# Optimization experiments

Hardware: AMD Instinct MI355X
Metric: run time of the kernel (lower is better)

Reference implementation:

```python
import jax, jax.numpy as jnp
import numpy as np

N, E, D, H, C = 50000, 1600000, 128, 2, 32

def setup_inputs() -> dict:
    key = jax.random.key(0)
    ks = jax.random.split(key, 8)
    x = jax.random.normal(ks[0], (N, D), jnp.float32)
    edge_index = jax.random.randint(ks[1], (2, E), 0, N)
    intra_enrichment_weights = jax.random.uniform(ks[2], (E,), jnp.float32)
    W = jax.random.normal(ks[3], (D, H * C), jnp.float32) * (1.0 / np.sqrt(D))
    att_src = jax.random.normal(ks[4], (H, C), jnp.float32) * 0.1
    att_dst = jax.random.normal(ks[5], (H, C), jnp.float32) * 0.1
    bias = jnp.zeros((H * C,), jnp.float32)
    enrichment_scale = jnp.asarray(0.01, jnp.float32)
    return dict(x=x, edge_index=edge_index,
                intra_enrichment_weights=intra_enrichment_weights,
                W=W, att_src=att_src, att_dst=att_dst, bias=bias,
                enrichment_scale=enrichment_scale)

def reference(x, edge_index, intra_enrichment_weights, W, att_src, att_dst, bias, enrichment_scale):
    n = x.shape[0]
    xf = jax.nn.elu(x)                       # F.elu on input features
    h = (xf @ W).reshape(n, H, C)            # [N, heads, out]
    # GATConv default add_self_loops=True
    loop = jnp.arange(n, dtype=edge_index.dtype)
    src = jnp.concatenate([edge_index[0], loop])
    dst = jnp.concatenate([edge_index[1], loop])
    a_src = jnp.einsum('nhc,hc->nh', h, att_src)   # [N, H]
    a_dst = jnp.einsum('nhc,hc->nh', h, att_dst)
    alpha = jax.nn.leaky_relu(a_src[src] + a_dst[dst], 0.2)  # [E+N, H]
    # softmax over incoming edges per destination node
    m = jax.ops.segment_max(alpha, dst, num_segments=n)
    e = jnp.exp(alpha - m[dst])
    denom = jax.ops.segment_sum(e, dst, num_segments=n)
    p = e / denom[dst]                       # every node has a self-loop -> denom > 0
    out = jax.ops.segment_sum(h[src] * p[:, :, None], dst, num_segments=n)  # [N, H, C]
    out = out.reshape(n, H * C) + bias
    # enrichment bias (scatter-mean of per-edge weights over source nodes)
    s0 = edge_index[0]
    nw = jax.ops.segment_sum(intra_enrichment_weights, s0, num_segments=n)
    cnt = jax.ops.segment_sum(jnp.ones_like(intra_enrichment_weights), s0, num_segments=n)
    nw = nw / jnp.maximum(cnt, 1.0)
    nw = jnp.clip(nw, 0.2, 5.0)
    scale_factor = 0.1 * jax.nn.sigmoid(enrichment_scale)
    return out + scale_factor * (nw[:, None] - 1.0)
```

## Files before the change

kernel.cpp:

```cpp
#include <hip/hip_runtime.h>


typedef unsigned int u32;
typedef unsigned short u16;

#define SLOTS 4864
#define NB_MAX 400
#define EPB 4096

#define XS 136
#define CS 68

typedef __attribute__((ext_vector_type(8))) short short8;
typedef __attribute__((ext_vector_type(4))) float float4v;

__device__ __forceinline__ u16 f2bf(float f) {
    union { float f; u32 u; } v; v.f = f;
    u32 r = v.u + 0x7fffu + ((v.u >> 16) & 1u);
    return (u16)(r >> 16);
}
__device__ __forceinline__ float bf2f(u16 u) {
    union { u32 i; float f; } v; v.i = ((u32)u) << 16; return v.f;
}
__device__ __forceinline__ float bf_lo(u32 u) {
    union { u32 i; float f; } v; v.i = u << 16; return v.f;
}
__device__ __forceinline__ float bf_hi(u32 u) {
    union { u32 i; float f; } v; v.i = u & 0xFFFF0000u; return v.f;
}
__device__ __forceinline__ void bf_split(float v, short& hi, short& lo) {
    u16 h = f2bf(v);
    float hf = bf2f(h);
    hi = (short)h;
    lo = (short)f2bf(v - hf);
}

__global__ void k_init(int* cursA, int* cursB, int nb) {
    int t = threadIdx.x;
    if (t < nb) { cursA[t] = 0; cursB[t] = 0; }
}

__global__ __launch_bounds__(256) void k_node(
    const float* __restrict__ x, const float* __restrict__ Wm,
    const float* __restrict__ att_s, const float* __restrict__ att_d,
    u32* __restrict__ hb32, float* __restrict__ a_src, float* __restrict__ a_dst,
    int nN)
{
    __shared__ __align__(16) short Ah[64 * XS];
    __shared__ __align__(16) short Al[64 * XS];
    __shared__ __align__(16) short Bh[64 * XS];
    __shared__ __align__(16) short Bl[64 * XS];
    float* Cl = (float*)Ah;

    int t = threadIdx.x;
    int n0 = blockIdx.x * 64;

    {
        int f = t & 63, kq = t >> 6;
        for (int kk = 0; kk < 32; ++kk) {
            int k = kq * 32 + kk;
            float wv = Wm[k * 64 + f];
            short hi, lo; bf_split(wv, hi, lo);
            Bh[f * XS + k] = hi; Bl[f * XS + k] = lo;
        }
    }
    for (int j = 0; j < 8; ++j) {
        int idx = t + 256 * j;
        int r = idx >> 5, c4 = idx & 31;
        int gn = n0 + r;
        float4 xv = make_float4(0.f, 0.f, 0.f, 0.f);
        if (gn < nN) xv = ((const float4*)x)[(size_t)gn * 32 + c4];
        float e[4];
        e[0] = xv.x > 0.f ? xv.x : expm1f(xv.x);
        e[1] = xv.y > 0.f ? xv.y : expm1f(xv.y);
        e[2] = xv.z > 0.f ? xv.z : expm1f(xv.z);
        e[3] = xv.w > 0.f ? xv.w : expm1f(xv.w);
        short h4[4], l4[4];
#pragma unroll
        for (int i = 0; i < 4; ++i) bf_split(e[i], h4[i], l4[i]);
        *(short4*)&Ah[r * XS + c4 * 4] = make_short4(h4[0], h4[1], h4[2], h4[3]);
        *(short4*)&Al[r * XS + c4 * 4] = make_short4(l4[0], l4[1], l4[2], l4[3]);
    }
    __syncthreads();

    {
        int w = t >> 6, l = t & 63;
        int q = l >> 4, m = l & 15;
        int arow = w * 16 + m;
        float4v acc[4] = {};
#pragma unroll
        for (int ks = 0; ks < 4; ++ks) {
            int k0 = ks * 32 + q * 8;
            short8 ah = *(const short8*)&Ah[arow * XS + k0];
            short8 al = *(const short8*)&Al[arow * XS + k0];
#pragma unroll
            for (int nt = 0; nt < 4; ++nt) {
                short8 bh = *(const short8*)&Bh[(nt * 16 + m) * XS + k0];
                short8 bl = *(const short8*)&Bl[(nt * 16 + m) * XS + k0];
                acc[nt] = __builtin_amdgcn_mfma_f32_16x16x32_bf16(ah, bh, acc[nt], 0, 0, 0);
                acc[nt] = __builtin_amdgcn_mfma_f32_16x16x32_bf16(ah, bl, acc[nt], 0, 0, 0);
                acc[nt] = __builtin_amdgcn_mfma_f32_16x16x32_bf16(al, bh, acc[nt], 0, 0, 0);
            }
        }
        __syncthreads();
#pragma unroll
        for (int nt = 0; nt < 4; ++nt)
#pragma unroll
            for (int r = 0; r < 4; ++r)
                Cl[(w * 16 + q * 4 + r) * CS + nt * 16 + m] = acc[nt][r];
    }
    __syncthreads();

    {
        int nl = t >> 2, fq = t & 3;
        int gn = n0 + nl;
        float ps = 0.f, pd = 0.f;
        if (gn < nN) {
            float hv[16];
#pragma unroll
            for (int i = 0; i < 16; ++i) {
                int f = fq * 16 + i;
                hv[i] = Cl[nl * CS + f];
                ps = fmaf(hv[i], att_s[f], ps);
                pd = fmaf(hv[i], att_d[f], pd);
            }
#pragma unroll
            for (int i = 0; i < 8; ++i) {
                u32 pk = ((u32)f2bf(hv[2 * i + 1]) << 16) | (u32)f2bf(hv[2 * i]);
                hb32[(size_t)gn * 32 + fq * 8 + i] = pk;
            }
        }
        float ps2 = ps + __shfl_xor(ps, 1, 64);
        float pd2 = pd + __shfl_xor(pd, 1, 64);
        if (gn < nN && (fq & 1) == 0) {
            a_src[2 * gn + (fq >> 1)] = ps2;
            a_dst[2 * gn + (fq >> 1)] = pd2;
        }
    }
}

__global__ __launch_bounds__(256) void k_partA(
    const int* __restrict__ ei, const float* __restrict__ wgt,
    int* cursA, int* cursB, u32* bufA, u32* bufB, int E, int nb)
{
    __shared__ u32 arrA[EPB], arrB[EPB];
    __shared__ u16 bkA[EPB], bkB[EPB];
    __shared__ int cntA[NB_MAX], cntB[NB_MAX];
    __shared__ int lofsA[NB_MAX], lofsB[NB_MAX];
    __shared__ int basA[NB_MAX], basB[NB_MAX];
    __shared__ int part[256];

    int t = threadIdx.x;
    for (int b = t; b < nb; b += 256) { cntA[b] = 0; cntB[b] = 0; }
    __syncthreads();

    int base = blockIdx.x * EPB;
    int nv = min(EPB, E - base);
    int sv[16], dv[16]; float wv[16];
#pragma unroll
    for (int k = 0; k < 16; ++k) {
        int e = base + k * 256 + t;
        if (e < E) { sv[k] = ei[e]; dv[k] = ei[E + e]; wv[k] = wgt[e]; }
        else       { sv[k] = -1;    dv[k] = -1;        wv[k] = 0.f; }
    }
#pragma unroll
    for (int k = 0; k < 16; ++k) {
        if (dv[k] >= 0) {
            atomicAdd(&cntA[dv[k] >> 7], 1);
            atomicAdd(&cntB[sv[k] >> 7], 1);
        }
    }
    __syncthreads();
    for (int b = t; b < nb; b += 256) {
        int ca = cntA[b], cb = cntB[b];
        if (ca > 0) basA[b] = atomicAdd(&cursA[b], ca);
        if (cb > 0) basB[b] = atomicAdd(&cursB[b], cb);
    }
    __syncthreads();
    {
        int b0 = 2 * t, b1 = 2 * t + 1;
        int c0 = (b0 < nb) ? cntA[b0] : 0;
        int c1 = (b1 < nb) ? cntA[b1] : 0;
        part[t] = c0 + c1;
        __syncthreads();
        for (int off = 1; off < 256; off <<= 1) {
            int v = (t >= off) ? part[t - off] : 0;
            __syncthreads();
            part[t] += v;
            __syncthreads();
        }
        int excl = part[t] - (c0 + c1);
        if (b0 < nb) lofsA[b0] = excl;
        if (b1 < nb) lofsA[b1] = excl + c0;
        __syncthreads();
        c0 = (b0 < nb) ? cntB[b0] : 0;
        c1 = (b1 < nb) ? cntB[b1] : 0;
        part[t] = c0 + c1;
        __syncthreads();
        for (int off = 1; off < 256; off <<= 1) {
            int v = (t >= off) ? part[t - off] : 0;
            __syncthreads();
            part[t] += v;
            __syncthreads();
        }
        excl = part[t] - (c0 + c1);
        if (b0 < nb) lofsB[b0] = excl;
        if (b1 < nb) lofsB[b1] = excl + c0;
    }
    __syncthreads();
    for (int b = t; b < nb; b += 256) { cntA[b] = 0; cntB[b] = 0; }
    __syncthreads();
#pragma unroll
    for (int k = 0; k < 16; ++k) {
        if (dv[k] >= 0) {
            int bA = dv[k] >> 7;
            int r = lofsA[bA] + atomicAdd(&cntA[bA], 1);
            arrA[r] = ((u32)(dv[k] & 127) << 16) | (u32)sv[k];
            bkA[r] = (u16)bA;
            int bB = sv[k] >> 7;
            u32 wf = (u32)(wv[k] * 16777216.f);
            if (wf > 0xFFFFFFu) wf = 0xFFFFFFu;
            int r2 = lofsB[bB] + atomicAdd(&cntB[bB], 1);
            arrB[r2] = ((u32)(sv[k] & 127) << 24) | wf;
            bkB[r2] = (u16)bB;
        }
    }
    __syncthreads();
    for (int i = t; i < nv; i += 256) {
        int bA = bkA[i];
        int g = basA[bA] + (i - lofsA[bA]);
        if (g < SLOTS) bufA[bA * SLOTS + g] = arrA[i];
    }
    for (int i = t; i < nv; i += 256) {
        int bB = bkB[i];
        int g = basB[bB] + (i - lofsB[bB]);
        if (g < SLOTS) bufB[bB * SLOTS + g] = arrB[i];
    }
}

__global__ __launch_bounds__(256) void k_partB_dst(
    const u32* bufA_in, const int* __restrict__ cursA,
    u32* bufA_out, int* __restrict__ deg, int* __restrict__ offs, int nN)
{
    __shared__ u32 st[SLOTS];
    __shared__ u32 st2[SLOTS];
    __shared__ int ldeg[128], lscan[128], lcur[128];
    int b = blockIdx.x, t = threadIdx.x;
    int n = cursA[b]; if (n > SLOTS) n = SLOTS;
    if (t < 128) { ldeg[t] = 0; lcur[t] = 0; }
    __syncthreads();
    for (int i = t; i < n; i += 256) {
        u32 v = bufA_in[b * SLOTS + i];
        st[i] = v;
        atomicAdd(&ldeg[v >> 16], 1);
    }
    __syncthreads();
    if (t < 128) lscan[t] = ldeg[t];
    __syncthreads();
    for (int off = 1; off < 128; off <<= 1) {
        int v = 0;
        if (t < 128 && t >= off) v = lscan[t - off];
        __syncthreads();
        if (t < 128) lscan[t] += v;
        __syncthreads();
    }
    int excl = 0;
    if (t < 128) excl = lscan[t] - ldeg[t];
    __syncthreads();
    if (t < 128) lscan[t] = excl;
    __syncthreads();
    for (int i = t; i < n; i += 256) {
        u32 v = st[i];
        int dl = v >> 16;
        int pos = lscan[dl] + atomicAdd(&lcur[dl], 1);
        st2[pos] = v & 0xFFFFu;
    }
    __syncthreads();
    for (int i = t; i < n; i += 256) bufA_out[b * SLOTS + i] = st2[i];
    int node = (b << 7) + t;
    if (t < 128 && node < nN) { deg[node] = ldeg[t]; offs[node] = b * SLOTS + lscan[t]; }
}

__global__ __launch_bounds__(256) void k_partB_src(
    const u32* __restrict__ bufB, const int* __restrict__ cursB,
    float* __restrict__ nwv, int nN)
{
    __shared__ u32 usum[128]; __shared__ int ucnt[128];
    int b = blockIdx.x, t = threadIdx.x;
    int n = cursB[b]; if (n > SLOTS) n = SLOTS;
    if (t < 128) { usum[t] = 0; ucnt[t] = 0; }
    __syncthreads();
    for (int i = t; i < n; i += 256) {
        u32 v = bufB[b * SLOTS + i];
        atomicAdd(&usum[v >> 24], v & 0xFFFFFFu);
        atomicAdd(&ucnt[v >> 24], 1);
    }
    __syncthreads();
    int node = (b << 7) + t;
    if (t < 128 && node < nN) {
        float cnt = (float)ucnt[t];
        float nw = ((float)usum[t] * (1.f / 16777216.f)) / fmaxf(cnt, 1.f);
        nwv[node] = fminf(fmaxf(nw, 0.2f), 5.f);
    }
}

__global__ __launch_bounds__(256) void k_accum(
    const u32* __restrict__ hb32,
    const float* __restrict__ a_src, const float* __restrict__ a_dst,
    const u32* __restrict__ esrc, const int* __restrict__ offs,
    const int* __restrict__ deg, const float* __restrict__ nwv,
    const float* __restrict__ bias, const float* __restrict__ esc,
    float* __restrict__ out, int nN)
{
    __shared__ u32 lds[4][2][64][2];
    int tid = threadIdx.x;
    int lane = tid & 63;
    int n = (blockIdx.x * 256 + tid) >> 6;
    if (n >= nN) return;
    int ws = tid >> 6;
    int l31 = lane & 31;
    int half = lane >> 5;
    int head = l31 >> 4;

    float ad0 = a_dst[2 * n], ad1 = a_dst[2 * n + 1];
    float as0 = a_src[2 * n], as1 = a_src[2 * n + 1];
    float t0 = as0 + ad0; t0 = t0 > 0.f ? t0 : 0.2f * t0;
    float t1 = as1 + ad1; t1 = t1 > 0.f ? t1 : 0.2f * t1;
    float es0 = __expf(t0), es1 = __expf(t1);

    u32 hself = hb32[(size_t)n * 32 + l31];
    float eself = head ? es1 : es0;
    float acc0 = half ? 0.f : eself * bf_lo(hself);
    float acc1 = half ? 0.f : eself * bf_hi(hself);
    float dsum0 = 0.f, dsum1 = 0.f;

    int start = offs[n], len = deg[n];
    for (int b0 = 0; b0 < len; b0 += 64) {
        int cnt = min(64, len - b0);
        u32 si = (u32)n; float e0 = 0.f, e1 = 0.f;
        if (lane < cnt) {
            si = esrc[start + b0 + lane];
            float2 ap = ((const float2*)a_src)[si];
            float v0 = ap.x + ad0; v0 = v0 > 0.f ? v0 : 0.2f * v0;
            float v1 = ap.y + ad1; v1 = v1 > 0.f ? v1 : 0.2f * v1;
            e0 = __expf(v0); e1 = __expf(v1);
        }
        dsum0 += e0; dsum1 += e1;
        lds[ws][0][lane][0] = si; lds[ws][0][lane][1] = __float_as_uint(e0);
        lds[ws][1][lane][0] = si; lds[ws][1][lane][1] = __float_as_uint(e1);

        int iters = (cnt + 1) >> 1;
#pragma unroll 4
        for (int k = 0; k < iters; ++k) {
            int e = 2 * k + half;
            u32 rsi = lds[ws][head][e][0];
            float w = __uint_as_float(lds[ws][head][e][1]);
            u32 hv = hb32[(size_t)rsi * 32 + l31];
            acc0 = fmaf(w, bf_lo(hv), acc0);
            acc1 = fmaf(w, bf_hi(hv), acc1);
        }
    }

#pragma unroll
    for (int off = 1; off < 64; off <<= 1) {
        dsum0 += __shfl_xor(dsum0, off, 64);
        dsum1 += __shfl_xor(dsum1, off, 64);
    }
    float den0 = es0 + dsum0, den1 = es1 + dsum1;

    acc0 += __shfl_xor(acc0, 32, 64);
    acc1 += __shfl_xor(acc1, 32, 64);

    if (half == 0) {
        float den = head ? den1 : den0;
        float sf = 0.1f / (1.f + __expf(-esc[0]));
        float en = sf * (nwv[n] - 1.f);
        float2 bb = ((const float2*)bias)[l31];
        float2 o;
        o.x = acc0 / den + bb.x + en;
        o.y = acc1 / den + bb.y + en;
        ((float2*)out)[(size_t)n * 32 + l31] = o;
    }
}

extern "C" void kernel_launch(void* const* d_in, const int* in_sizes, int n_in,
                              void* d_out, int out_size, void* d_ws, size_t ws_size,
                              hipStream_t stream)
{
    const float* x     = (const float*)d_in[0];
    const int*   ei    = (const int*)d_in[1];
    const float* wgt   = (const float*)d_in[2];
    const float* Wm    = (const float*)d_in[3];
    const float* att_s = (const float*)d_in[4];
    const float* att_d = (const float*)d_in[5];
    const float* bias  = (const float*)d_in[6];
    const float* esc   = (const float*)d_in[7];
    float* out = (float*)d_out;

    int nN = in_sizes[0] / 128;
    int E  = in_sizes[2];
    int NB = (nN + 127) / 128;

    char* p = (char*)d_ws;
    auto alloc = [&](size_t bytes) -> char* {
        char* r = p; p += (bytes + 255) & ~(size_t)255; return r;
    };
    u32*   hb32  = (u32*)  alloc((size_t)nN * 32 * 4);
    float* a_src = (float*)alloc((size_t)nN * 2 * 4);
    float* a_dst = (float*)alloc((size_t)nN * 2 * 4);
    int*   deg   = (int*)  alloc((size_t)nN * 4);
    int*   offs  = (int*)  alloc((size_t)nN * 4);
    float* nwv   = (float*)alloc((size_t)nN * 4);
    int*   cursA = (int*)  alloc(NB_MAX * 4);
    int*   cursB = (int*)  alloc(NB_MAX * 4);
    u32*   bufA  = (u32*)  alloc((size_t)NB * SLOTS * 4);
    u32*   bufB  = (u32*)  alloc((size_t)NB * SLOTS * 4);

    int nblkA = (E + EPB - 1) / EPB;

    k_init<<<dim3(1), dim3(512), 0, stream>>>(cursA, cursB, NB);
    k_node<<<dim3((nN + 63) / 64), dim3(256), 0, stream>>>(x, Wm, att_s, att_d, hb32, a_src, a_dst, nN);
    k_partA<<<dim3(nblkA), dim3(256), 0, stream>>>(ei, wgt, cursA, cursB, bufA, bufB, E, NB);
    k_partB_dst<<<dim3(NB), dim3(256), 0, stream>>>(bufA, cursA, bufA, deg, offs, nN);
    k_partB_src<<<dim3(NB), dim3(256), 0, stream>>>(bufB, cursB, nwv, nN);
    k_accum<<<dim3((nN + 3) / 4), dim3(256), 0, stream>>>(hb32, a_src, a_dst, bufA, offs, deg,
                                                          nwv, bias, esc, out, nN);
}
```

Before: 193.9 us.

## Precompute fp16 edge weights in bucketing pass and simplify accumulation loop

Bucket width drops from 128 to 64 nodes, which lets partA pack the full node id in the record and drop the per-slot bucket arrays. The two partB kernels merge into one. That kernel now computes the exp(leaky_relu) attention weights per edge, stores them as fp16 pairs in a 64-bit record next to the source id, and sorts by destination. The accumulation kernel then streams these records directly instead of staging them in LDS and recomputing the exponentials, and it drops the full wave reduction of the denominator. Costs are an extra 8-byte-per-edge buffer, fp16 weight precision, 16-bit enrichment weight quantisation, and more buckets with tighter slot capacity.

```diff
diff --git a/kernel.cpp b/kernel.cpp
--- a/kernel.cpp
+++ b/kernel.cpp
@@ -1,12 +1,14 @@
 #include <hip/hip_runtime.h>
+#include <hip/hip_fp16.h>
 
 
 typedef unsigned int u32;
 typedef unsigned short u16;
-
-#define SLOTS 4864
-#define NB_MAX 400
-#define EPB 4096
+typedef unsigned long long u64;
+
+#define SLOTS 2432
+#define NBMAX 800
+#define EPB 2048
 
 #define XS 136
 #define CS 68
@@ -34,10 +36,18 @@
     hi = (short)h;
     lo = (short)f2bf(v - hf);
 }
+__device__ __forceinline__ u16 f2h(float f) {
+    __half h = __float2half(f);
+    return *(u16*)&h;
+}
+__device__ __forceinline__ float h2f(u16 u) {
+    __half h = *(__half*)&u;
+    return __half2float(h);
+}
 
 __global__ void k_init(int* cursA, int* cursB, int nb) {
-    int t = threadIdx.x;
-    if (t < nb) { cursA[t] = 0; cursB[t] = 0; }
+    int i = blockIdx.x * blockDim.x + threadIdx.x;
+    if (i < nb) { cursA[i] = 0; cursB[i] = 0; }
 }
 
 __global__ __launch_bounds__(256) void k_node(
@@ -144,10 +154,9 @@
     int* cursA, int* cursB, u32* bufA, u32* bufB, int E, int nb)
 {
     __shared__ u32 arrA[EPB], arrB[EPB];
-    __shared__ u16 bkA[EPB], bkB[EPB];
-    __shared__ int cntA[NB_MAX], cntB[NB_MAX];
-    __shared__ int lofsA[NB_MAX], lofsB[NB_MAX];
-    __shared__ int basA[NB_MAX], basB[NB_MAX];
+    __shared__ int cntA[NBMAX], cntB[NBMAX];
+    __shared__ int lofsA[NBMAX], lofsB[NBMAX];
+    __shared__ int basA[NBMAX], basB[NBMAX];
     __shared__ int part[256];
 
     int t = threadIdx.x;
@@ -156,18 +165,18 @@
 
     int base = blockIdx.x * EPB;
     int nv = min(EPB, E - base);
-    int sv[16], dv[16]; float wv[16];
-#pragma unroll
-    for (int k = 0; k < 16; ++k) {
+    int sv[8], dv[8]; float wv[8];
+#pragma unroll
+    for (int k = 0; k < 8; ++k) {
         int e = base + k * 256 + t;
         if (e < E) { sv[k] = ei[e]; dv[k] = ei[E + e]; wv[k] = wgt[e]; }
         else       { sv[k] = -1;    dv[k] = -1;        wv[k] = 0.f; }
     }
 #pragma unroll
-    for (int k = 0; k < 16; ++k) {
+    for (int k = 0; k < 8; ++k) {
         if (dv[k] >= 0) {
-            atomicAdd(&cntA[dv[k] >> 7], 1);
-            atomicAdd(&cntB[sv[k] >> 7], 1);
+            atomicAdd(&cntA[dv[k] >> 6], 1);
+            atomicAdd(&cntB[sv[k] >> 6], 1);
         }
     }
     __syncthreads();
@@ -178,10 +187,13 @@
     }
     __syncthreads();
     {
-        int b0 = 2 * t, b1 = 2 * t + 1;
-        int c0 = (b0 < nb) ? cntA[b0] : 0;
-        int c1 = (b1 < nb) ? cntA[b1] : 0;
-        part[t] = c0 + c1;
+        int c[4]; int s = 0;
+#pragma unroll
+        for (int j = 0; j < 4; ++j) {
+            int b = 4 * t + j;
+            c[j] = (b < nb) ? cntA[b] : 0; s += c[j];
+        }
+        part[t] = s;
         __syncthreads();
         for (int off = 1; off < 256; off <<= 1) {
             int v = (t >= off) ? part[t - off] : 0;
@@ -189,13 +201,21 @@
             part[t] += v;
             __syncthreads();
         }
-        int excl = part[t] - (c0 + c1);
-        if (b0 < nb) lofsA[b0] = excl;
-        if (b1 < nb) lofsA[b1] = excl + c0;
-        __syncthreads();
-        c0 = (b0 < nb) ? cntB[b0] : 0;
-        c1 = (b1 < nb) ? cntB[b1] : 0;
-        part[t] = c0 + c1;
+        int ex = part[t] - s;
+#pragma unroll
+        for (int j = 0; j < 4; ++j) {
+            int b = 4 * t + j;
+            if (b < nb) lofsA[b] = ex;
+            ex += c[j];
+        }
+        __syncthreads();
+        s = 0;
+#pragma unroll
+        for (int j = 0; j < 4; ++j) {
+            int b = 4 * t + j;
+            c[j] = (b < nb) ? cntB[b] : 0; s += c[j];
+        }
+        part[t] = s;
         __syncthreads();
         for (int off = 1; off < 256; off <<= 1) {
             int v = (t >= off) ? part[t - off] : 0;
@@ -203,129 +223,146 @@
             part[t] += v;
             __syncthreads();
         }
-        excl = part[t] - (c0 + c1);
-        if (b0 < nb) lofsB[b0] = excl;
-        if (b1 < nb) lofsB[b1] = excl + c0;
+        ex = part[t] - s;
+#pragma unroll
+        for (int j = 0; j < 4; ++j) {
+            int b = 4 * t + j;
+            if (b < nb) lofsB[b] = ex;
+            ex += c[j];
+        }
     }
     __syncthreads();
     for (int b = t; b < nb; b += 256) { cntA[b] = 0; cntB[b] = 0; }
     __syncthreads();
 #pragma unroll
-    for (int k = 0; k < 16; ++k) {
+    for (int k = 0; k < 8; ++k) {
         if (dv[k] >= 0) {
-            int bA = dv[k] >> 7;
+            int bA = dv[k] >> 6;
             int r = lofsA[bA] + atomicAdd(&cntA[bA], 1);
-            arrA[r] = ((u32)(dv[k] & 127) << 16) | (u32)sv[k];
-            bkA[r] = (u16)bA;
-            int bB = sv[k] >> 7;
-            u32 wf = (u32)(wv[k] * 16777216.f);
-            if (wf > 0xFFFFFFu) wf = 0xFFFFFFu;
+            arrA[r] = ((u32)dv[k] << 16) | (u32)sv[k];
+            int bB = sv[k] >> 6;
+            u32 wf = (u32)(wv[k] * 65535.f);
+            if (wf > 0xFFFFu) wf = 0xFFFFu;
             int r2 = lofsB[bB] + atomicAdd(&cntB[bB], 1);
-            arrB[r2] = ((u32)(sv[k] & 127) << 24) | wf;
-            bkB[r2] = (u16)bB;
+            arrB[r2] = ((u32)sv[k] << 16) | wf;
         }
     }
     __syncthreads();
     for (int i = t; i < nv; i += 256) {
-        int bA = bkA[i];
+        u32 v = arrA[i];
+        int bA = v >> 22;
         int g = basA[bA] + (i - lofsA[bA]);
-        if (g < SLOTS) bufA[bA * SLOTS + g] = arrA[i];
+        if (g < SLOTS) bufA[bA * SLOTS + g] = v;
     }
     for (int i = t; i < nv; i += 256) {
-        int bB = bkB[i];
+        u32 v = arrB[i];
+        int bB = v >> 22;
         int g = basB[bB] + (i - lofsB[bB]);
-        if (g < SLOTS) bufB[bB * SLOTS + g] = arrB[i];
-    }
-}
-
-__global__ __launch_bounds__(256) void k_partB_dst(
-    const u32* bufA_in, const int* __restrict__ cursA,
-    u32* bufA_out, int* __restrict__ deg, int* __restrict__ offs, int nN)
-{
-    __shared__ u32 st[SLOTS];
-    __shared__ u32 st2[SLOTS];
-    __shared__ int ldeg[128], lscan[128], lcur[128];
-    int b = blockIdx.x, t = threadIdx.x;
-    int n = cursA[b]; if (n > SLOTS) n = SLOTS;
-    if (t < 128) { ldeg[t] = 0; lcur[t] = 0; }
-    __syncthreads();
-    for (int i = t; i < n; i += 256) {
-        u32 v = bufA_in[b * SLOTS + i];
-        st[i] = v;
-        atomicAdd(&ldeg[v >> 16], 1);
-    }
-    __syncthreads();
-    if (t < 128) lscan[t] = ldeg[t];
-    __syncthreads();
-    for (int off = 1; off < 128; off <<= 1) {
-        int v = 0;
-        if (t < 128 && t >= off) v = lscan[t - off];
-        __syncthreads();
-        if (t < 128) lscan[t] += v;
-        __syncthreads();
-    }
-    int excl = 0;
-    if (t < 128) excl = lscan[t] - ldeg[t];
-    __syncthreads();
-    if (t < 128) lscan[t] = excl;
-    __syncthreads();
-    for (int i = t; i < n; i += 256) {
-        u32 v = st[i];
-        int dl = v >> 16;
-        int pos = lscan[dl] + atomicAdd(&lcur[dl], 1);
-        st2[pos] = v & 0xFFFFu;
-    }
-    __syncthreads();
-    for (int i = t; i < n; i += 256) bufA_out[b * SLOTS + i] = st2[i];
-    int node = (b << 7) + t;
-    if (t < 128 && node < nN) { deg[node] = ldeg[t]; offs[node] = b * SLOTS + lscan[t]; }
-}
-
-__global__ __launch_bounds__(256) void k_partB_src(
+        if (g < SLOTS) bufB[bB * SLOTS + g] = v;
+    }
+}
+
+__global__ __launch_bounds__(256) void k_partB(
+    const u32* __restrict__ bufA, const int* __restrict__ cursA,
     const u32* __restrict__ bufB, const int* __restrict__ cursB,
+    const float* __restrict__ a_src, const float* __restrict__ a_dst,
+    u64* __restrict__ grp, int* __restrict__ deg, int* __restrict__ offs,
     float* __restrict__ nwv, int nN)
 {
-    __shared__ u32 usum[128]; __shared__ int ucnt[128];
+    __shared__ u32 stv[SLOTS];
+    __shared__ u32 s2a[SLOTS], s2b[SLOTS];
+    __shared__ int ldeg[64], lscan[64], lcur[64];
+    __shared__ float add0[64], add1[64];
+    __shared__ u32 usum[64]; __shared__ int ucnt[64];
+
     int b = blockIdx.x, t = threadIdx.x;
-    int n = cursB[b]; if (n > SLOTS) n = SLOTS;
-    if (t < 128) { usum[t] = 0; ucnt[t] = 0; }
-    __syncthreads();
-    for (int i = t; i < n; i += 256) {
+    int nA = cursA[b]; if (nA > SLOTS) nA = SLOTS;
+
+    if (t < 64) {
+        ldeg[t] = 0; lcur[t] = 0;
+        int node = (b << 6) + t;
+        float2 ad = make_float2(0.f, 0.f);
+        if (node < nN) ad = ((const float2*)a_dst)[node];
+        add0[t] = ad.x; add1[t] = ad.y;
+    }
+    __syncthreads();
+    for (int i = t; i < nA; i += 256) {
+        u32 v = bufA[b * SLOTS + i];
+        stv[i] = v;
+        atomicAdd(&ldeg[(v >> 16) & 63], 1);
+    }
+    __syncthreads();
+    if (t < 64) lscan[t] = ldeg[t];
+    __syncthreads();
+    for (int off = 1; off < 64; off <<= 1) {
+        int v = 0;
+        if (t < 64 && t >= off) v = lscan[t - off];
+        __syncthreads();
+        if (t < 64) lscan[t] += v;
+        __syncthreads();
+    }
+    int ex = 0;
+    if (t < 64) ex = lscan[t] - ldeg[t];
+    __syncthreads();
+    if (t < 64) lscan[t] = ex;
+    __syncthreads();
+    for (int i = t; i < nA; i += 256) {
+        u32 v = stv[i];
+        int s = v & 0xFFFF;
+        int dl = (v >> 16) & 63;
+        float2 ap = ((const float2*)a_src)[s];
+        float v0 = ap.x + add0[dl]; v0 = v0 > 0.f ? v0 : 0.2f * v0;
+        float v1 = ap.y + add1[dl]; v1 = v1 > 0.f ? v1 : 0.2f * v1;
+        u32 wp = ((u32)f2h(__expf(v1)) << 16) | (u32)f2h(__expf(v0));
+        int pos = lscan[dl] + atomicAdd(&lcur[dl], 1);
+        s2a[pos] = (u32)s;
+        s2b[pos] = wp;
+    }
+    __syncthreads();
+    for (int i = t; i < nA; i += 256)
+        grp[(size_t)b * SLOTS + i] = ((u64)s2b[i] << 32) | s2a[i];
+    if (t < 64) {
+        int node = (b << 6) + t;
+        if (node < nN) { deg[node] = ldeg[t]; offs[node] = b * SLOTS + lscan[t]; }
+        usum[t] = 0; ucnt[t] = 0;
+    }
+    __syncthreads();
+    int nB = cursB[b]; if (nB > SLOTS) nB = SLOTS;
+    for (int i = t; i < nB; i += 256) {
         u32 v = bufB[b * SLOTS + i];
-        atomicAdd(&usum[v >> 24], v & 0xFFFFFFu);
-        atomicAdd(&ucnt[v >> 24], 1);
-    }
-    __syncthreads();
-    int node = (b << 7) + t;
-    if (t < 128 && node < nN) {
-        float cnt = (float)ucnt[t];
-        float nw = ((float)usum[t] * (1.f / 16777216.f)) / fmaxf(cnt, 1.f);
-        nwv[node] = fminf(fmaxf(nw, 0.2f), 5.f);
+        atomicAdd(&usum[(v >> 16) & 63], v & 0xFFFFu);
+        atomicAdd(&ucnt[(v >> 16) & 63], 1);
+    }
+    __syncthreads();
+    if (t < 64) {
+        int node = (b << 6) + t;
+        if (node < nN) {
+            float cnt = (float)ucnt[t];
+            float nw = ((float)usum[t] * (1.f / 65535.f)) / fmaxf(cnt, 1.f);
+            nwv[node] = fminf(fmaxf(nw, 0.2f), 5.f);
+        }
     }
 }
 
 __global__ __launch_bounds__(256) void k_accum(
-    const u32* __restrict__ hb32,
+    const u32* __restrict__ hb32, const u64* __restrict__ grp,
     const float* __restrict__ a_src, const float* __restrict__ a_dst,
-    const u32* __restrict__ esrc, const int* __restrict__ offs,
-    const int* __restrict__ deg, const float* __restrict__ nwv,
-    const float* __restrict__ bias, const float* __restrict__ esc,
-    float* __restrict__ out, int nN)
+    const int* __restrict__ offs, const int* __restrict__ deg,
+    const float* __restrict__ nwv, const float* __restrict__ bias,
+    const float* __restrict__ esc, float* __restrict__ out, int nN)
 {
-    __shared__ u32 lds[4][2][64][2];
     int tid = threadIdx.x;
     int lane = tid & 63;
     int n = (blockIdx.x * 256 + tid) >> 6;
     if (n >= nN) return;
-    int ws = tid >> 6;
     int l31 = lane & 31;
     int half = lane >> 5;
     int head = l31 >> 4;
 
-    float ad0 = a_dst[2 * n], ad1 = a_dst[2 * n + 1];
-    float as0 = a_src[2 * n], as1 = a_src[2 * n + 1];
-    float t0 = as0 + ad0; t0 = t0 > 0.f ? t0 : 0.2f * t0;
-    float t1 = as1 + ad1; t1 = t1 > 0.f ? t1 : 0.2f * t1;
+    float2 asn = ((const float2*)a_src)[n];
+    float2 adn = ((const float2*)a_dst)[n];
+    float t0 = asn.x + adn.x; t0 = t0 > 0.f ? t0 : 0.2f * t0;
+    float t1 = asn.y + adn.y; t1 = t1 > 0.f ? t1 : 0.2f * t1;
     float es0 = __expf(t0), es1 = __expf(t1);
 
     u32 hself = hb32[(size_t)n * 32 + l31];
@@ -335,41 +372,28 @@
     float dsum0 = 0.f, dsum1 = 0.f;
 
     int start = offs[n], len = deg[n];
-    for (int b0 = 0; b0 < len; b0 += 64) {
-        int cnt = min(64, len - b0);
-        u32 si = (u32)n; float e0 = 0.f, e1 = 0.f;
-        if (lane < cnt) {
-            si = esrc[start + b0 + lane];
-            float2 ap = ((const float2*)a_src)[si];
-            float v0 = ap.x + ad0; v0 = v0 > 0.f ? v0 : 0.2f * v0;
-            float v1 = ap.y + ad1; v1 = v1 > 0.f ? v1 : 0.2f * v1;
-            e0 = __expf(v0); e1 = __expf(v1);
-        }
-        dsum0 += e0; dsum1 += e1;
-        lds[ws][0][lane][0] = si; lds[ws][0][lane][1] = __float_as_uint(e0);
-        lds[ws][1][lane][0] = si; lds[ws][1][lane][1] = __float_as_uint(e1);
-
-        int iters = (cnt + 1) >> 1;
+    int iters = (len + 1) >> 1;
 #pragma unroll 4
-        for (int k = 0; k < iters; ++k) {
-            int e = 2 * k + half;
-            u32 rsi = lds[ws][head][e][0];
-            float w = __uint_as_float(lds[ws][head][e][1]);
-            u32 hv = hb32[(size_t)rsi * 32 + l31];
-            acc0 = fmaf(w, bf_lo(hv), acc0);
-            acc1 = fmaf(w, bf_hi(hv), acc1);
-        }
-    }
-
-#pragma unroll
-    for (int off = 1; off < 64; off <<= 1) {
-        dsum0 += __shfl_xor(dsum0, off, 64);
-        dsum1 += __shfl_xor(dsum1, off, 64);
-    }
+    for (int k = 0; k < iters; ++k) {
+        int e = 2 * k + half;
+        u64 rec = grp[start + e];
+        u32 si = (u32)rec & 0xFFFFu;
+        u32 wp = (u32)(rec >> 32);
+        float w0 = h2f((u16)(wp & 0xFFFFu));
+        float w1 = h2f((u16)(wp >> 16));
+        if (e >= len) { w0 = 0.f; w1 = 0.f; }
+        u32 hv = hb32[(size_t)si * 32 + l31];
+        float ws = head ? w1 : w0;
+        acc0 = fmaf(ws, bf_lo(hv), acc0);
+        acc1 = fmaf(ws, bf_hi(hv), acc1);
+        dsum0 += w0; dsum1 += w1;
+    }
+
+    dsum0 += __shfl_xor(dsum0, 32, 64);
+    dsum1 += __shfl_xor(dsum1, 32, 64);
+    acc0  += __shfl_xor(acc0, 32, 64);
+    acc1  += __shfl_xor(acc1, 32, 64);
     float den0 = es0 + dsum0, den1 = es1 + dsum1;
-
-    acc0 += __shfl_xor(acc0, 32, 64);
-    acc1 += __shfl_xor(acc1, 32, 64);
 
     if (half == 0) {
         float den = head ? den1 : den0;
@@ -399,7 +423,7 @@
 
     int nN = in_sizes[0] / 128;
     int E  = in_sizes[2];
-    int NB = (nN + 127) / 128;
+    int NB = (nN + 63) / 64;
 
     char* p = (char*)d_ws;
     auto alloc = [&](size_t bytes) -> char* {
@@ -411,18 +435,19 @@
     int*   deg   = (int*)  alloc((size_t)nN * 4);
     int*   offs  = (int*)  alloc((size_t)nN * 4);
     float* nwv   = (float*)alloc((size_t)nN * 4);
-    int*   cursA = (int*)  alloc(NB_MAX * 4);
-    int*   cursB = (int*)  alloc(NB_MAX * 4);
+    int*   cursA = (int*)  alloc(NBMAX * 4);
+    int*   cursB = (int*)  alloc(NBMAX * 4);
     u32*   bufA  = (u32*)  alloc((size_t)NB * SLOTS * 4);
     u32*   bufB  = (u32*)  alloc((size_t)NB * SLOTS * 4);
+    u64*   grp   = (u64*)  alloc(((size_t)NB * SLOTS + 64) * 8);
 
     int nblkA = (E + EPB - 1) / EPB;
 
-    k_init<<<dim3(1), dim3(512), 0, stream>>>(cursA, cursB, NB);
+    k_init<<<dim3((NB + 255) / 256), dim3(256), 0, stream>>>(cursA, cursB, NB);
     k_node<<<dim3((nN + 63) / 64), dim3(256), 0, stream>>>(x, Wm, att_s, att_d, hb32, a_src, a_dst, nN);
     k_partA<<<dim3(nblkA), dim3(256), 0, stream>>>(ei, wgt, cursA, cursB, bufA, bufB, E, NB);
-    k_partB_dst<<<dim3(NB), dim3(256), 0, stream>>>(bufA, cursA, bufA, deg, offs, nN);
-    k_partB_src<<<dim3(NB), dim3(256), 0, stream>>>(bufB, cursB, nwv, nN);
-    k_accum<<<dim3((nN + 3) / 4), dim3(256), 0, stream>>>(hb32, a_src, a_dst, bufA, offs, deg,
+    k_partB<<<dim3(NB), dim3(256), 0, stream>>>(bufA, cursA, bufB, cursB, a_src, a_dst,
+                                                grp, deg, offs, nwv, nN);
+    k_accum<<<dim3((nN + 3) / 4), dim3(256), 0, stream>>>(hb32, grp, a_src, a_dst, offs, deg,
                                                           nwv, bias, esc, out, nN);
 }
```

Result: slower. 219.9 us (+13.4%).
